# Performance work log

Hardware: AMD Instinct MI355X
Metric: run time of the kernel (lower is better)

Reference implementation:

```python
import jax, jax.numpy as jnp
import numpy as np

N, H, V, MAX_STEPS = 256, 128, 64, 4

def setup_inputs() -> dict:
    key = jax.random.key(0)
    ks = jax.random.split(key, 16)
    def w(k, shape, fan_in):
        return jax.random.normal(k, shape, dtype=jnp.float32) / np.sqrt(fan_in)
    inp = {}
    inp['node_embeddings'] = jax.random.normal(ks[0], (N, H), dtype=jnp.float32)
    inp['skip_embeddings'] = jax.random.normal(ks[1], (N, N, H), dtype=jnp.float32)
    inp['Wx'] = w(ks[2], (H, 4 * H), H)
    inp['Wh'] = w(ks[3], (H, 4 * H), H)
    inp['b'] = jnp.zeros((4 * H,), jnp.float32)
    inp['Wxs'] = w(ks[4], (H, 4 * H), H)
    inp['Whs'] = w(ks[5], (H, 4 * H), H)
    inp['bs'] = jnp.zeros((4 * H,), jnp.float32)
    inp['Wb'] = w(ks[6], (2 * H, 2), 2 * H)
    inp['bb'] = jnp.zeros((2,), jnp.float32)
    inp['Wk'] = w(ks[7], (H, H), H)
    inp['bk'] = jnp.zeros((H,), jnp.float32)
    inp['Wq'] = w(ks[8], (2 * H, H), 2 * H)
    inp['bq'] = jnp.zeros((H,), jnp.float32)
    inp['Wl'] = w(ks[9], (2 * H, 1), 2 * H)
    inp['bl'] = jnp.zeros((1,), jnp.float32)
    inp['Wd'] = w(ks[10], (2 * H, V), 2 * H)
    inp['bd'] = jnp.zeros((V,), jnp.float32)
    # valid skips only forward in the program (include diagonal = no-skip)
    inp['skip_mask'] = jnp.triu(jnp.ones((N, N), dtype=bool))
    inp['true_indexes'] = jax.random.randint(ks[11], (N,), 0, N, dtype=jnp.int32)
    inp['false_indexes'] = jax.random.randint(ks[12], (N,), 0, N, dtype=jnp.int32)
    inp['exit_index'] = N - 1
    return inp

def _lstm(c, h, x, Wx, Wh, b):
    gates = x @ Wx + h @ Wh + b  # [..., 4H]
    i, f, g, o = jnp.split(gates, 4, axis=-1)
    c2 = jax.nn.sigmoid(f) * c + jax.nn.sigmoid(i) * jnp.tanh(g)
    h2 = jax.nn.sigmoid(o) * jnp.tanh(c2)
    return c2, h2

def reference(node_embeddings, skip_embeddings, Wx, Wh, b, Wxs, Whs, bs,
              Wb, bb, Wk, bk, Wq, bq, Wl, bl, Wd, bd,
              skip_mask, true_indexes, false_indexes, exit_index):
    n, hdim = node_embeddings.shape
    eye = jnp.eye(n, dtype=node_embeddings.dtype)
    ip0 = jnp.zeros((n,), node_embeddings.dtype).at[0].set(1.0)
    c0 = jnp.zeros((n, hdim), node_embeddings.dtype)
    h0 = jnp.zeros((n, hdim), node_embeddings.dtype)
    keys = skip_embeddings @ Wk + bk  # [N,N,H] (input-only, precompute)

    def step(carry, _):
        ip, c, h = carry
        # per-node LSTM proposals
        c_p, h_p = _lstm(c, h, node_embeddings, Wx, Wh, b)  # [N,H]
        hid = jnp.concatenate([c_p, h_p], axis=-1)  # [N,2H]
        # skip proposals: carry of source i applied to skip embedding (i,j)
        c_sk, h_sk = _lstm(c[:, None, :], h[:, None, :], skip_embeddings, Wxs, Whs, bs)  # [N,N,H]
        # branch decisions
        branch = jax.nn.softmax(hid @ Wb + bb, axis=-1)  # [N,2]
        # skip decisions (per source i, softmax over destinations j)
        queries = hid @ Wq + bq  # [N,H]
        kq = jax.nn.relu(jnp.concatenate(
            [keys, jnp.broadcast_to(queries[:, None, :], (n, n, hdim))], axis=-1))  # [N,N,2H]
        logits = jnp.einsum('ijk,kl->ijl', kq, Wl)[..., 0] + bl[0]  # [N,N]
        skip_dec = jax.nn.softmax(jnp.where(skip_mask, logits, -jnp.inf), axis=-1)
        # aggregation (IPA)
        yes_skip = skip_dec * (1.0 - eye)  # zero diagonal
        no_skip = jnp.diagonal(skip_dec)
        p_bt = ip * no_skip * branch[:, 0]
        p_bf = ip * no_skip * branch[:, 1]
        new_ip = (jax.ops.segment_sum(p_bt, true_indexes, num_segments=n)
                  + jax.ops.segment_sum(p_bf, false_indexes, num_segments=n)
                  + jnp.einsum('i,ij->j', ip, yes_skip))
        denom = new_ip[:, None] + 1e-7
        def agg(hp, hsk):
            t = jax.ops.segment_sum(hp * p_bt[:, None], true_indexes, num_segments=n)
            f = jax.ops.segment_sum(hp * p_bf[:, None], false_indexes, num_segments=n)
            s = jnp.einsum('ijh,i,ij->jh', hsk, ip, yes_skip)
            return (t + f + s) / denom
        return (new_ip, agg(c_p, c_sk), agg(h_p, h_sk)), None

    (ip, c, h), _ = jax.lax.scan(step, (ip0, c0, h0), None, length=MAX_STEPS)
    exit_concat = jnp.concatenate([c[exit_index], h[exit_index]], axis=-1)  # [2H]
    return exit_concat @ Wd + bd  # [V]
```

## Files before the change

### kernel.cpp

```cpp
#include <hip/hip_runtime.h>
#include <hip/hip_bf16.h>

constexpr int NN = 256;
constexpr int HH = 128;
constexpr int GG = 512;
constexpr int NP = NN * NN;
constexpr int NCH = 8;
constexpr int CHSZ = 32;

typedef __attribute__((ext_vector_type(8))) short short8;
typedef __attribute__((ext_vector_type(4))) float f32x4;

__device__ unsigned short g_xs[(size_t)NP * GG];
__device__ unsigned short g_wfr[20 * 512 * 8];
__device__ float g_bsp[GG];
__device__ float g_pwh[HH * HH * 4];
__device__ float g_pws[HH * HH * 4];
__device__ float g_kterm[NP];
__device__ float g_yeswT[NP];
__device__ float g_noskip[NN];
__device__ float g_xg[NN * HH * 4];
__device__ float g_xga[NN * HH * 4];
__device__ float g_hws[NN * HH * 4];
__device__ float g_c[NN * HH];
__device__ float g_h[NN * HH];
__device__ float g_sc[NN * HH];
__device__ float g_sh[NN * HH];
__device__ float g_pc[NCH * NN * HH];
__device__ float g_ph[NCH * NN * HH];
__device__ float g_pw[NCH * NN];
__device__ float g_ip[NN];
__device__ float g_nip[NN];

__device__ __forceinline__ unsigned short f2bf(float f) {
  unsigned int u = __float_as_uint(f);
  u = (u + 0x7fffu + ((u >> 16) & 1u)) >> 16;
  return (unsigned short)u;
}
__device__ __forceinline__ float bf2f(unsigned short s) {
  return __uint_as_float(((unsigned int)s) << 16);
}
__device__ __forceinline__ float frcp(float x) {
#if __has_builtin(__builtin_amdgcn_rcpf)
  return __builtin_amdgcn_rcpf(x);
#else
  return 1.0f / x;
#endif
}
__device__ __forceinline__ float sigm(float x) { return frcp(1.f + __expf(-x)); }
__device__ __forceinline__ float tanhfast(float x) { return 1.f - 2.f * frcp(__expf(2.f * x) + 1.f); }

__global__ __launch_bounds__(512) void k_pre(const float* __restrict__ NE,
                                             const float* __restrict__ Wx,
                                             const float* __restrict__ b,
                                             const float* __restrict__ Wxs,
                                             const float* __restrict__ Wk,
                                             const float* __restrict__ bs,
                                             const float* __restrict__ Wh,
                                             const float* __restrict__ Whs) {
  const int bid = blockIdx.x;
  const int tid = threadIdx.x;
  if (bid < 64) {
    const int idx = bid * 512 + tid;
    g_sc[idx] = 0.f; g_sh[idx] = 0.f; g_c[idx] = 0.f; g_h[idx] = 0.f;
    *(float4*)&g_hws[(size_t)idx * 4] = make_float4(0.f, 0.f, 0.f, 0.f);
    if (idx < NN) { g_nip[idx] = 0.f; g_ip[idx] = (idx == 0) ? 1.f : 0.f; }
  } else if (bid < 84) {
    const int bidx = bid - 64;
    const int tile = bidx >> 2, ks = bidx & 3;
    const int ct = tid >> 6, l = tid & 63;
    const int c = ct * 16 + (l & 15);
    const int kbase = ks * 32 + (l >> 4) * 8;
    int src = 0;
    if (tile < 4) src = (c & 3) * 128 + tile * 32 + (c >> 2);
    unsigned short* dst = &g_wfr[((size_t)bidx * 512 + tid) * 8];
#pragma unroll
    for (int e = 0; e < 8; ++e) {
      int k = kbase + e;
      float v = (tile < 4) ? Wxs[k * GG + src] : Wk[k * HH + c];
      dst[e] = f2bf(v);
    }
    if (tile < 4 && ks == 0 && (l >> 4) == 0) g_bsp[tile * 128 + c] = bs[src];
  } else if (bid < 116) {
    const int k = (bid - 84) * 4 + (tid >> 7), t = tid & 127;
    float4 a = make_float4(Wh[k * GG + t], Wh[k * GG + 128 + t], Wh[k * GG + 256 + t], Wh[k * GG + 384 + t]);
    float4 s = make_float4(Whs[k * GG + t], Whs[k * GG + 128 + t], Whs[k * GG + 256 + t], Whs[k * GG + 384 + t]);
    *(float4*)&g_pwh[((size_t)k * HH + t) * 4] = a;
    *(float4*)&g_pws[((size_t)k * HH + t) * 4] = s;
  } else {
    __shared__ float ne[4][HH];
    const int sub = tid >> 7, t = tid & 127;
    const int i = (bid - 116) * 4 + sub;
    ne[sub][t] = NE[i * HH + t];
    __syncthreads();
    float a0 = b[t], a1 = b[128 + t], a2 = b[256 + t], a3 = b[384 + t];
    for (int k = 0; k < HH; ++k) {
      float x = ne[sub][k];
      a0 = fmaf(x, Wx[k * GG + t], a0);
      a1 = fmaf(x, Wx[k * GG + 128 + t], a1);
      a2 = fmaf(x, Wx[k * GG + 256 + t], a2);
      a3 = fmaf(x, Wx[k * GG + 384 + t], a3);
    }
    float4 v = make_float4(a0, a1, a2, a3);
    *(float4*)&g_xg[((size_t)i * HH + t) * 4] = v;
    *(float4*)&g_xga[((size_t)i * HH + t) * 4] = v;
  }
}

__device__ __forceinline__ void loadB(short8* dst, int tile, int ks, int l) {
  const unsigned short* wf = &g_wfr[((size_t)(tile * 4 + ks)) * 4096 + l * 8];
#pragma unroll
  for (int ct = 0; ct < 8; ++ct) dst[ct] = *(const short8*)(wf + ct * 512);
}

__global__ __launch_bounds__(256) void k_gemm(const float* __restrict__ SE,
                                              const float* __restrict__ bk,
                                              const float* __restrict__ Wl) {
  __shared__ __align__(16) char lds[32768];
  const int bid = blockIdx.x;
  const int tile = blockIdx.y;
  const int pb = (bid < 128) ? (bid * 2) : ((bid - 128) * 2 + 1);
  const int pairBase = pb * 128;
  const int tid = threadIdx.x;

  for (int cc = tid; cc < 2048; cc += 256) {
    int row = cc >> 4, kc = cc & 15;
    const float* src = SE + (size_t)(pairBase + row) * HH + kc * 8;
    float4 f0 = *(const float4*)(src);
    float4 f1 = *(const float4*)(src + 4);
    short8 v;
    v[0] = (short)f2bf(f0.x); v[1] = (short)f2bf(f0.y); v[2] = (short)f2bf(f0.z); v[3] = (short)f2bf(f0.w);
    v[4] = (short)f2bf(f1.x); v[5] = (short)f2bf(f1.y); v[6] = (short)f2bf(f1.z); v[7] = (short)f2bf(f1.w);
    *(short8*)(lds + row * 256 + ((kc * 16) ^ ((row & 7) << 4))) = v;
  }
  __syncthreads();

  const int wv = tid >> 6;
  const int l = tid & 63;
  const int l15 = l & 15, lg = l >> 4;

  f32x4 acc[2][8];
#pragma unroll
  for (int rt = 0; rt < 2; ++rt)
#pragma unroll
    for (int ct = 0; ct < 8; ++ct) acc[rt][ct] = (f32x4){0.f, 0.f, 0.f, 0.f};

  short8 bA[8], bB[8];
  loadB(bA, tile, 0, l);
#pragma unroll
  for (int ks = 0; ks < 4; ks += 2) {
    loadB(bB, tile, ks + 1, l);
    {
      const int kb = ks * 64 + lg * 16;
      short8 a[2];
#pragma unroll
      for (int rt = 0; rt < 2; ++rt) {
        int row = wv * 32 + rt * 16 + l15;
        a[rt] = *(const short8*)(lds + row * 256 + (kb ^ ((row & 7) << 4)));
      }
#pragma unroll
      for (int rt = 0; rt < 2; ++rt)
#pragma unroll
        for (int ct = 0; ct < 8; ++ct)
          acc[rt][ct] = __builtin_amdgcn_mfma_f32_16x16x32_bf16(a[rt], bA[ct], acc[rt][ct], 0, 0, 0);
    }
    if (ks + 2 < 4) loadB(bA, tile, ks + 2, l);
    {
      const int kb = (ks + 1) * 64 + lg * 16;
      short8 a[2];
#pragma unroll
      for (int rt = 0; rt < 2; ++rt) {
        int row = wv * 32 + rt * 16 + l15;
        a[rt] = *(const short8*)(lds + row * 256 + (kb ^ ((row & 7) << 4)));
      }
#pragma unroll
      for (int rt = 0; rt < 2; ++rt)
#pragma unroll
        for (int ct = 0; ct < 8; ++ct)
          acc[rt][ct] = __builtin_amdgcn_mfma_f32_16x16x32_bf16(a[rt], bB[ct], acc[rt][ct], 0, 0, 0);
    }
  }

  if (tile < 4) {
#pragma unroll
    for (int rt = 0; rt < 2; ++rt)
#pragma unroll
      for (int ct = 0; ct < 8; ++ct) {
        const int col = ct * 16 + l15;
        const float bsv = g_bsp[tile * 128 + col];
#pragma unroll
        for (int r = 0; r < 4; ++r) {
          int row = wv * 32 + rt * 16 + lg * 4 + r;
          int pair = pairBase + row;
          int jj = pair & 255, ii = pair >> 8;
          if (jj > ii)
            g_xs[((size_t)jj * NN + ii) * GG + tile * 128 + col] = f2bf(acc[rt][ct][r] + bsv);
        }
      }
  } else {
#pragma unroll
    for (int rt = 0; rt < 2; ++rt) {
#pragma unroll
      for (int r = 0; r < 4; ++r) {
        float s = 0.f;
#pragma unroll
        for (int ct = 0; ct < 8; ++ct) {
          int col = ct * 16 + l15;
          float x = acc[rt][ct][r] + bk[col];
          x = fmaxf(x, 0.f);
          s = fmaf(x, Wl[col], s);
        }
#pragma unroll
        for (int m = 1; m < 16; m <<= 1) s += __shfl_xor(s, m, 64);
        int row = wv * 32 + rt * 16 + lg * 4 + r;
        int pair = pairBase + row;
        int jj = pair & 255, ii = pair >> 8;
        if (l15 == 0 && jj >= ii) g_kterm[pair] = s;
      }
    }
  }
}

__global__ __launch_bounds__(256) void k_softmax() {
  const int i = blockIdx.x, j = threadIdx.x;
  __shared__ float sm[NN];
  float x = -1e30f;
  if (j >= i) x = g_kterm[i * NN + j];
  sm[j] = x;
  __syncthreads();
  for (int s = 128; s > 0; s >>= 1) { if (j < s) sm[j] = fmaxf(sm[j], sm[j + s]); __syncthreads(); }
  float mx = sm[0];
  __syncthreads();
  float e = (j >= i) ? __expf(x - mx) : 0.f;
  sm[j] = e;
  __syncthreads();
  for (int s = 128; s > 0; s >>= 1) { if (j < s) sm[j] += sm[j + s]; __syncthreads(); }
  float p = e * frcp(sm[0]);
  g_yeswT[j * NN + i] = (j == i) ? 0.f : p;
  if (j == i) g_noskip[i] = p;
}

__global__ __launch_bounds__(128) void k_step(const float* __restrict__ Wb,
                                              const float* __restrict__ bb,
                                              const int* __restrict__ tix,
                                              const int* __restrict__ fix) {
  const int t = threadIdx.x;
  if (blockIdx.x < 256) {
    const int i = blockIdx.x;
    __shared__ float red[2][2];
    const float4 a = *(const float4*)&g_xga[((size_t)i * HH + t) * 4];
    float co = g_c[i * HH + t];
    float c2 = sigm(a.y) * co + sigm(a.x) * tanhfast(a.z);
    float h2 = sigm(a.w) * tanhfast(c2);
    float q0 = c2 * Wb[2 * t] + h2 * Wb[2 * (128 + t)];
    float q1 = c2 * Wb[2 * t + 1] + h2 * Wb[2 * (128 + t) + 1];
#pragma unroll
    for (int m = 1; m < 64; m <<= 1) { q0 += __shfl_xor(q0, m, 64); q1 += __shfl_xor(q1, m, 64); }
    if ((t & 63) == 0) { red[t >> 6][0] = q0; red[t >> 6][1] = q1; }
    __syncthreads();
    float l0 = red[0][0] + red[1][0] + bb[0];
    float l1 = red[0][1] + red[1][1] + bb[1];
    float mm = fmaxf(l0, l1);
    float e0 = __expf(l0 - mm), e1 = __expf(l1 - mm);
    float inv = frcp(e0 + e1);
    float ipv = g_ip[i] * g_noskip[i];
    if (ipv != 0.f) {
      float pbt = ipv * e0 * inv, pbf = ipv * e1 * inv;
      int ti = tix[i], fi = fix[i];
      atomicAdd(&g_sc[ti * HH + t], c2 * pbt);
      atomicAdd(&g_sh[ti * HH + t], h2 * pbt);
      atomicAdd(&g_sc[fi * HH + t], c2 * pbf);
      atomicAdd(&g_sh[fi * HH + t], h2 * pbf);
      if (t == 0) { atomicAdd(&g_nip[ti], pbt); atomicAdd(&g_nip[fi], pbf); }
    }
  } else {
    const int idx = blockIdx.x - 256;
    const int j = idx >> 3, ch = idx & 7;
    const int i0 = ch * CHSZ;
    if (i0 >= j) return;
    const int iN = (j - i0 < CHSZ) ? (j - i0) : CHSZ;
    __shared__ float wsh[CHSZ];
    if (t < CHSZ) wsh[t] = (t < iN) ? g_ip[i0 + t] * g_yeswT[j * NN + i0 + t] : 0.f;
    __syncthreads();
    float accC = 0.f, accH = 0.f, accW = 0.f;
    for (int ii = 0; ii < iN; ++ii) {
      float wgt = wsh[ii];
      if (wgt == 0.f) continue;
      const int i = i0 + ii;
      const ushort4 gv = *(const ushort4*)&g_xs[((size_t)j * NN + i) * GG + t * 4];
      float4 hw = *(const float4*)&g_hws[((size_t)i * HH + t) * 4];
      float xi = bf2f(gv.x) + hw.x;
      float xf = bf2f(gv.y) + hw.y;
      float xg = bf2f(gv.z) + hw.z;
      float xo = bf2f(gv.w) + hw.w;
      float c2 = sigm(xf) * g_c[i * HH + t] + sigm(xi) * tanhfast(xg);
      float h2 = sigm(xo) * tanhfast(c2);
      accC = fmaf(wgt, c2, accC);
      accH = fmaf(wgt, h2, accH);
      accW += wgt;
    }
    g_pc[((size_t)ch * NN + j) * HH + t] = accC;
    g_ph[((size_t)ch * NN + j) * HH + t] = accH;
    if (t == 0) g_pw[ch * NN + j] = accW;
  }
}

__global__ __launch_bounds__(256) void k_finish(const int last) {
  const int j0 = blockIdx.x * 4;
  const int tid = threadIdx.x;
  __shared__ float hsm[4][HH];
  __shared__ float nipsh[4];
  if (tid < 4) {
    const int j = j0 + tid;
    float nip = g_nip[j];
    const int nch = (j + 31) >> 5;
    for (int ch = 0; ch < nch; ++ch) nip += g_pw[ch * NN + j];
    nipsh[tid] = nip;
    g_ip[j] = nip;
    g_nip[j] = 0.f;
  }
  __syncthreads();
#pragma unroll
  for (int s = 0; s < 2; ++s) {
    const int slot = tid + s * 256;
    const int jj = slot >> 7, t = slot & 127;
    const int j = j0 + jj;
    float sc = g_sc[j * HH + t], sh = g_sh[j * HH + t];
    const int nch = (j + 31) >> 5;
    for (int ch = 0; ch < nch; ++ch) {
      sc += g_pc[((size_t)ch * NN + j) * HH + t];
      sh += g_ph[((size_t)ch * NN + j) * HH + t];
    }
    float d = frcp(nipsh[jj] + 1e-7f);
    float cv = sc * d, hv = sh * d;
    g_c[j * HH + t] = cv;
    g_h[j * HH + t] = hv;
    hsm[jj][t] = hv;
    g_sc[j * HH + t] = 0.f;
    g_sh[j * HH + t] = 0.f;
  }
  __syncthreads();
  if (last) return;
  const int m = tid >> 7, t = tid & 127;
  const float* __restrict__ W = m ? g_pws : g_pwh;
  float4 a0 = make_float4(0.f, 0.f, 0.f, 0.f), a1 = a0, a2 = a0, a3 = a0;
#pragma unroll 4
  for (int k = 0; k < HH; ++k) {
    const float4 w = *(const float4*)&W[((size_t)k * HH + t) * 4];
    const float h0 = hsm[0][k], h1 = hsm[1][k], h2 = hsm[2][k], h3 = hsm[3][k];
    a0.x = fmaf(h0, w.x, a0.x); a0.y = fmaf(h0, w.y, a0.y); a0.z = fmaf(h0, w.z, a0.z); a0.w = fmaf(h0, w.w, a0.w);
    a1.x = fmaf(h1, w.x, a1.x); a1.y = fmaf(h1, w.y, a1.y); a1.z = fmaf(h1, w.z, a1.z); a1.w = fmaf(h1, w.w, a1.w);
    a2.x = fmaf(h2, w.x, a2.x); a2.y = fmaf(h2, w.y, a2.y); a2.z = fmaf(h2, w.z, a2.z); a2.w = fmaf(h2, w.w, a2.w);
    a3.x = fmaf(h3, w.x, a3.x); a3.y = fmaf(h3, w.y, a3.y); a3.z = fmaf(h3, w.z, a3.z); a3.w = fmaf(h3, w.w, a3.w);
  }
  if (m == 0) {
    float4 x0 = *(const float4*)&g_xg[((size_t)(j0 + 0) * HH + t) * 4];
    float4 x1 = *(const float4*)&g_xg[((size_t)(j0 + 1) * HH + t) * 4];
    float4 x2 = *(const float4*)&g_xg[((size_t)(j0 + 2) * HH + t) * 4];
    float4 x3 = *(const float4*)&g_xg[((size_t)(j0 + 3) * HH + t) * 4];
    *(float4*)&g_xga[((size_t)(j0 + 0) * HH + t) * 4] = make_float4(x0.x + a0.x, x0.y + a0.y, x0.z + a0.z, x0.w + a0.w);
    *(float4*)&g_xga[((size_t)(j0 + 1) * HH + t) * 4] = make_float4(x1.x + a1.x, x1.y + a1.y, x1.z + a1.z, x1.w + a1.w);
    *(float4*)&g_xga[((size_t)(j0 + 2) * HH + t) * 4] = make_float4(x2.x + a2.x, x2.y + a2.y, x2.z + a2.z, x2.w + a2.w);
    *(float4*)&g_xga[((size_t)(j0 + 3) * HH + t) * 4] = make_float4(x3.x + a3.x, x3.y + a3.y, x3.z + a3.z, x3.w + a3.w);
  } else {
    *(float4*)&g_hws[((size_t)(j0 + 0) * HH + t) * 4] = a0;
    *(float4*)&g_hws[((size_t)(j0 + 1) * HH + t) * 4] = a1;
    *(float4*)&g_hws[((size_t)(j0 + 2) * HH + t) * 4] = a2;
    *(float4*)&g_hws[((size_t)(j0 + 3) * HH + t) * 4] = a3;
  }
}

__global__ __launch_bounds__(64) void k_out(const float* __restrict__ Wd,
                                            const float* __restrict__ bd,
                                            const int* __restrict__ ei,
                                            float* __restrict__ out) {
  const int v = threadIdx.x;
  const int e = ei[0];
  float s = bd[v];
  for (int h = 0; h < HH; ++h) {
    s = fmaf(g_c[e * HH + h], Wd[h * 64 + v], s);
    s = fmaf(g_h[e * HH + h], Wd[(128 + h) * 64 + v], s);
  }
  out[v] = s;
}

extern "C" void kernel_launch(void* const* d_in, const int* in_sizes, int n_in,
                              void* d_out, int out_size, void* d_ws, size_t ws_size,
                              hipStream_t stream) {
  const float* NE  = (const float*)d_in[0];
  const float* SE  = (const float*)d_in[1];
  const float* Wx  = (const float*)d_in[2];
  const float* Wh  = (const float*)d_in[3];
  const float* b   = (const float*)d_in[4];
  const float* Wxs = (const float*)d_in[5];
  const float* Whs = (const float*)d_in[6];
  const float* bs  = (const float*)d_in[7];
  const float* Wb  = (const float*)d_in[8];
  const float* bb  = (const float*)d_in[9];
  const float* Wk  = (const float*)d_in[10];
  const float* bk  = (const float*)d_in[11];
  const float* Wl  = (const float*)d_in[14];
  const float* Wd  = (const float*)d_in[16];
  const float* bd  = (const float*)d_in[17];
  const int* tix = (const int*)d_in[19];
  const int* fix = (const int*)d_in[20];
  const int* ei  = (const int*)d_in[21];
  float* out = (float*)d_out;

  k_pre<<<180, 512, 0, stream>>>(NE, Wx, b, Wxs, Wk, bs, Wh, Whs);
  k_gemm<<<dim3(384, 5), 256, 0, stream>>>(SE, bk, Wl);
  k_softmax<<<256, 256, 0, stream>>>();
  for (int s = 0; s < 4; ++s) {
    k_step<<<256 + NN * NCH, 128, 0, stream>>>(Wb, bb, tix, fix);
    k_finish<<<64, 256, 0, stream>>>(s == 3);
  }
  k_out<<<1, 64, 0, stream>>>(Wd, bd, ei, out);
}
```

Before: 179.7 us.

## Pre-convert skip embeddings to bf16, DMA into LDS, atomic skip aggregation, split finish

The fp32-to-bf16 conversion of skip embeddings moves into k_pre, which writes a pre-swizzled bf16 buffer. k_gemm then loads it straight into LDS with global_load_lds instead of converting per block. The skip-aggregation partials are now atomically added into g_sc/g_sh/g_nip using 4 chunks of 64 instead of 8 partial buffers. k_finish is split into a normalise kernel and a separate 256-block recurrent-matmul kernel that uses more parallelism. In exchange this adds an extra pass over 32 MB of embeddings, more atomic contention, and the zero-weight skip test is removed.

```diff
diff --git a/kernel.cpp b/kernel.cpp
--- a/kernel.cpp
+++ b/kernel.cpp
@@ -5,13 +5,14 @@
 constexpr int HH = 128;
 constexpr int GG = 512;
 constexpr int NP = NN * NN;
-constexpr int NCH = 8;
-constexpr int CHSZ = 32;
+constexpr int NCH = 4;
+constexpr int CHSZ = 64;
 
 typedef __attribute__((ext_vector_type(8))) short short8;
 typedef __attribute__((ext_vector_type(4))) float f32x4;
 
 __device__ unsigned short g_xs[(size_t)NP * GG];
+__device__ unsigned short g_sebf[(size_t)NP * HH];
 __device__ unsigned short g_wfr[20 * 512 * 8];
 __device__ float g_bsp[GG];
 __device__ float g_pwh[HH * HH * 4];
@@ -26,9 +27,6 @@
 __device__ float g_h[NN * HH];
 __device__ float g_sc[NN * HH];
 __device__ float g_sh[NN * HH];
-__device__ float g_pc[NCH * NN * HH];
-__device__ float g_ph[NCH * NN * HH];
-__device__ float g_pw[NCH * NN];
 __device__ float g_ip[NN];
 __device__ float g_nip[NN];
 
@@ -57,7 +55,8 @@
                                              const float* __restrict__ Wk,
                                              const float* __restrict__ bs,
                                              const float* __restrict__ Wh,
-                                             const float* __restrict__ Whs) {
+                                             const float* __restrict__ Whs,
+                                             const float* __restrict__ SE) {
   const int bid = blockIdx.x;
   const int tid = threadIdx.x;
   if (bid < 64) {
@@ -87,7 +86,7 @@
     float4 s = make_float4(Whs[k * GG + t], Whs[k * GG + 128 + t], Whs[k * GG + 256 + t], Whs[k * GG + 384 + t]);
     *(float4*)&g_pwh[((size_t)k * HH + t) * 4] = a;
     *(float4*)&g_pws[((size_t)k * HH + t) * 4] = s;
-  } else {
+  } else if (bid < 180) {
     __shared__ float ne[4][HH];
     const int sub = tid >> 7, t = tid & 127;
     const int i = (bid - 116) * 4 + sub;
@@ -104,6 +103,20 @@
     float4 v = make_float4(a0, a1, a2, a3);
     *(float4*)&g_xg[((size_t)i * HH + t) * 4] = v;
     *(float4*)&g_xga[((size_t)i * HH + t) * 4] = v;
+  } else {
+    const int p0 = (bid - 180) * 256;
+    for (int e = tid; e < 4096; e += 512) {
+      const int pl = e >> 4, g = e & 15;
+      const int pair = p0 + pl;
+      const int gs = g ^ (pair & 7);
+      const float* src = SE + (size_t)pair * HH + gs * 8;
+      float4 f0 = *(const float4*)(src);
+      float4 f1 = *(const float4*)(src + 4);
+      short8 v;
+      v[0] = (short)f2bf(f0.x); v[1] = (short)f2bf(f0.y); v[2] = (short)f2bf(f0.z); v[3] = (short)f2bf(f0.w);
+      v[4] = (short)f2bf(f1.x); v[5] = (short)f2bf(f1.y); v[6] = (short)f2bf(f1.z); v[7] = (short)f2bf(f1.w);
+      *(short8*)&g_sebf[(size_t)pair * HH + g * 8] = v;
+    }
   }
 }
 
@@ -113,8 +126,7 @@
   for (int ct = 0; ct < 8; ++ct) dst[ct] = *(const short8*)(wf + ct * 512);
 }
 
-__global__ __launch_bounds__(256) void k_gemm(const float* __restrict__ SE,
-                                              const float* __restrict__ bk,
+__global__ __launch_bounds__(256) void k_gemm(const float* __restrict__ bk,
                                               const float* __restrict__ Wl) {
   __shared__ __align__(16) char lds[32768];
   const int bid = blockIdx.x;
@@ -123,15 +135,16 @@
   const int pairBase = pb * 128;
   const int tid = threadIdx.x;
 
-  for (int cc = tid; cc < 2048; cc += 256) {
-    int row = cc >> 4, kc = cc & 15;
-    const float* src = SE + (size_t)(pairBase + row) * HH + kc * 8;
-    float4 f0 = *(const float4*)(src);
-    float4 f1 = *(const float4*)(src + 4);
-    short8 v;
-    v[0] = (short)f2bf(f0.x); v[1] = (short)f2bf(f0.y); v[2] = (short)f2bf(f0.z); v[3] = (short)f2bf(f0.w);
-    v[4] = (short)f2bf(f1.x); v[5] = (short)f2bf(f1.y); v[6] = (short)f2bf(f1.z); v[7] = (short)f2bf(f1.w);
-    *(short8*)(lds + row * 256 + ((kc * 16) ^ ((row & 7) << 4))) = v;
+  {
+    const char* src = (const char*)g_sebf + (size_t)pairBase * 256;
+    const int wvoff = (tid >> 6) * 1024;
+#pragma unroll
+    for (int it = 0; it < 8; ++it) {
+      __builtin_amdgcn_global_load_lds(
+          (const __attribute__((address_space(1))) unsigned int*)(src + it * 4096 + tid * 16),
+          (__attribute__((address_space(3))) unsigned int*)(lds + it * 4096 + wvoff),
+          16, 0, 0);
+    }
   }
   __syncthreads();
 
@@ -275,17 +288,16 @@
     }
   } else {
     const int idx = blockIdx.x - 256;
-    const int j = idx >> 3, ch = idx & 7;
+    const int j = idx >> 2, ch = idx & 3;
     const int i0 = ch * CHSZ;
     if (i0 >= j) return;
     const int iN = (j - i0 < CHSZ) ? (j - i0) : CHSZ;
     __shared__ float wsh[CHSZ];
-    if (t < CHSZ) wsh[t] = (t < iN) ? g_ip[i0 + t] * g_yeswT[j * NN + i0 + t] : 0.f;
+    if (t < CHSZ) wsh[t] = g_ip[i0 + t] * g_yeswT[j * NN + i0 + t];
     __syncthreads();
     float accC = 0.f, accH = 0.f, accW = 0.f;
     for (int ii = 0; ii < iN; ++ii) {
-      float wgt = wsh[ii];
-      if (wgt == 0.f) continue;
+      const float wgt = wsh[ii];
       const int i = i0 + ii;
       const ushort4 gv = *(const ushort4*)&g_xs[((size_t)j * NN + i) * GG + t * 4];
       float4 hw = *(const float4*)&g_hws[((size_t)i * HH + t) * 4];
@@ -299,74 +311,57 @@
       accH = fmaf(wgt, h2, accH);
       accW += wgt;
     }
-    g_pc[((size_t)ch * NN + j) * HH + t] = accC;
-    g_ph[((size_t)ch * NN + j) * HH + t] = accH;
-    if (t == 0) g_pw[ch * NN + j] = accW;
-  }
-}
-
-__global__ __launch_bounds__(256) void k_finish(const int last) {
-  const int j0 = blockIdx.x * 4;
+    if (accW != 0.f) {
+      atomicAdd(&g_sc[j * HH + t], accC);
+      atomicAdd(&g_sh[j * HH + t], accH);
+      if (t == 0) atomicAdd(&g_nip[j], accW);
+    }
+  }
+}
+
+__global__ __launch_bounds__(512) void k_finA() {
   const int tid = threadIdx.x;
-  __shared__ float hsm[4][HH];
-  __shared__ float nipsh[4];
-  if (tid < 4) {
-    const int j = j0 + tid;
-    float nip = g_nip[j];
-    const int nch = (j + 31) >> 5;
-    for (int ch = 0; ch < nch; ++ch) nip += g_pw[ch * NN + j];
-    nipsh[tid] = nip;
-    g_ip[j] = nip;
-    g_nip[j] = 0.f;
-  }
-  __syncthreads();
-#pragma unroll
-  for (int s = 0; s < 2; ++s) {
-    const int slot = tid + s * 256;
-    const int jj = slot >> 7, t = slot & 127;
-    const int j = j0 + jj;
-    float sc = g_sc[j * HH + t], sh = g_sh[j * HH + t];
-    const int nch = (j + 31) >> 5;
-    for (int ch = 0; ch < nch; ++ch) {
-      sc += g_pc[((size_t)ch * NN + j) * HH + t];
-      sh += g_ph[((size_t)ch * NN + j) * HH + t];
-    }
-    float d = frcp(nipsh[jj] + 1e-7f);
-    float cv = sc * d, hv = sh * d;
-    g_c[j * HH + t] = cv;
-    g_h[j * HH + t] = hv;
-    hsm[jj][t] = hv;
-    g_sc[j * HH + t] = 0.f;
-    g_sh[j * HH + t] = 0.f;
-  }
-  __syncthreads();
-  if (last) return;
-  const int m = tid >> 7, t = tid & 127;
+  const int j = blockIdx.x * 4 + (tid >> 7), t = tid & 127;
+  float nip = g_nip[j];
+  float d = frcp(nip + 1e-7f);
+  g_c[j * HH + t] = g_sc[j * HH + t] * d;
+  g_h[j * HH + t] = g_sh[j * HH + t] * d;
+  g_sc[j * HH + t] = 0.f;
+  g_sh[j * HH + t] = 0.f;
+  if (t == 0) { g_ip[j] = nip; g_nip[j] = 0.f; }
+}
+
+__global__ __launch_bounds__(256) void k_finB() {
+  __shared__ float hsm[64 * 132];
+  __shared__ float wsmT[4 * 128];
+  const int b = blockIdx.x;
+  const int cg = b >> 1, m = b & 1;
+  const int tid = threadIdx.x;
   const float* __restrict__ W = m ? g_pws : g_pwh;
-  float4 a0 = make_float4(0.f, 0.f, 0.f, 0.f), a1 = a0, a2 = a0, a3 = a0;
-#pragma unroll 4
-  for (int k = 0; k < HH; ++k) {
-    const float4 w = *(const float4*)&W[((size_t)k * HH + t) * 4];
-    const float h0 = hsm[0][k], h1 = hsm[1][k], h2 = hsm[2][k], h3 = hsm[3][k];
-    a0.x = fmaf(h0, w.x, a0.x); a0.y = fmaf(h0, w.y, a0.y); a0.z = fmaf(h0, w.z, a0.z); a0.w = fmaf(h0, w.w, a0.w);
-    a1.x = fmaf(h1, w.x, a1.x); a1.y = fmaf(h1, w.y, a1.y); a1.z = fmaf(h1, w.z, a1.z); a1.w = fmaf(h1, w.w, a1.w);
-    a2.x = fmaf(h2, w.x, a2.x); a2.y = fmaf(h2, w.y, a2.y); a2.z = fmaf(h2, w.z, a2.z); a2.w = fmaf(h2, w.w, a2.w);
-    a3.x = fmaf(h3, w.x, a3.x); a3.y = fmaf(h3, w.y, a3.y); a3.z = fmaf(h3, w.z, a3.z); a3.w = fmaf(h3, w.w, a3.w);
-  }
-  if (m == 0) {
-    float4 x0 = *(const float4*)&g_xg[((size_t)(j0 + 0) * HH + t) * 4];
-    float4 x1 = *(const float4*)&g_xg[((size_t)(j0 + 1) * HH + t) * 4];
-    float4 x2 = *(const float4*)&g_xg[((size_t)(j0 + 2) * HH + t) * 4];
-    float4 x3 = *(const float4*)&g_xg[((size_t)(j0 + 3) * HH + t) * 4];
-    *(float4*)&g_xga[((size_t)(j0 + 0) * HH + t) * 4] = make_float4(x0.x + a0.x, x0.y + a0.y, x0.z + a0.z, x0.w + a0.w);
-    *(float4*)&g_xga[((size_t)(j0 + 1) * HH + t) * 4] = make_float4(x1.x + a1.x, x1.y + a1.y, x1.z + a1.z, x1.w + a1.w);
-    *(float4*)&g_xga[((size_t)(j0 + 2) * HH + t) * 4] = make_float4(x2.x + a2.x, x2.y + a2.y, x2.z + a2.z, x2.w + a2.w);
-    *(float4*)&g_xga[((size_t)(j0 + 3) * HH + t) * 4] = make_float4(x3.x + a3.x, x3.y + a3.y, x3.z + a3.z, x3.w + a3.w);
-  } else {
-    *(float4*)&g_hws[((size_t)(j0 + 0) * HH + t) * 4] = a0;
-    *(float4*)&g_hws[((size_t)(j0 + 1) * HH + t) * 4] = a1;
-    *(float4*)&g_hws[((size_t)(j0 + 2) * HH + t) * 4] = a2;
-    *(float4*)&g_hws[((size_t)(j0 + 3) * HH + t) * 4] = a3;
+  for (int e = tid; e < 512; e += 256) {
+    const int cc = e >> 7, k = e & 127;
+    wsmT[cc * 128 + k] = W[(size_t)k * 512 + cg * 4 + cc];
+  }
+  const int il = tid >> 2, cc = tid & 3;
+  for (int it = 0; it < 4; ++it) {
+    const int i0 = it * 64;
+    __syncthreads();
+    for (int e = tid; e < 2048; e += 256) {
+      const int r = e >> 5, kq = e & 31;
+      *(float4*)&hsm[r * 132 + kq * 4] = *(const float4*)&g_h[(size_t)(i0 + r) * HH + kq * 4];
+    }
+    __syncthreads();
+    float acc = 0.f;
+#pragma unroll 8
+    for (int k4 = 0; k4 < 32; ++k4) {
+      const float4 h4 = *(const float4*)&hsm[il * 132 + k4 * 4];
+      const float4 w4 = *(const float4*)&wsmT[cc * 128 + k4 * 4];
+      acc = fmaf(h4.x, w4.x, acc); acc = fmaf(h4.y, w4.y, acc);
+      acc = fmaf(h4.z, w4.z, acc); acc = fmaf(h4.w, w4.w, acc);
+    }
+    const size_t o = (size_t)(i0 + il) * 512 + cg * 4 + cc;
+    if (m == 0) g_xga[o] = g_xg[o] + acc;
+    else g_hws[o] = acc;
   }
 }
 
@@ -407,12 +402,13 @@
   const int* ei  = (const int*)d_in[21];
   float* out = (float*)d_out;
 
-  k_pre<<<180, 512, 0, stream>>>(NE, Wx, b, Wxs, Wk, bs, Wh, Whs);
-  k_gemm<<<dim3(384, 5), 256, 0, stream>>>(SE, bk, Wl);
+  k_pre<<<436, 512, 0, stream>>>(NE, Wx, b, Wxs, Wk, bs, Wh, Whs, SE);
+  k_gemm<<<dim3(384, 5), 256, 0, stream>>>(bk, Wl);
   k_softmax<<<256, 256, 0, stream>>>();
   for (int s = 0; s < 4; ++s) {
     k_step<<<256 + NN * NCH, 128, 0, stream>>>(Wb, bb, tix, fix);
-    k_finish<<<64, 256, 0, stream>>>(s == 3);
+    k_finA<<<64, 512, 0, stream>>>();
+    if (s != 3) k_finB<<<256, 256, 0, stream>>>();
   }
   k_out<<<1, 64, 0, stream>>>(Wd, bd, ei, out);
 }
```

Measured after the change: 182.1 us. Within noise of the previous version (+1.4%).
